# Kernel tuning notes

Measured on AMD Instinct MI355X. Metric: run time of the kernel, lower is better.

The kernel has to match this reference:

```python
import jax, jax.numpy as jnp
import numpy as np

GAMMA = 20.0
NUM_VIEWS = 64

def setup_inputs() -> dict:
    key = jax.random.key(0)
    k1, k2, k3 = jax.random.split(key, 3)
    B, L, D = 16, 4096, 1024
    v_pad = jax.random.normal(k1, (B, L, D), dtype=jnp.float32)
    v_len = jax.random.randint(k2, (B,), 1, L + 1, dtype=jnp.int32)
    # (T, H, W) per sample; only W/H ratio matters -> square 64x64 grid
    grid_thws = jnp.tile(jnp.array([[1, 64, 64]], dtype=jnp.int32), (B, 1))
    centers = jax.random.uniform(k3, (B, NUM_VIEWS, 2), dtype=jnp.float32)
    return {"v_pad": v_pad, "v_len": v_len, "grid_thws": grid_thws, "centers": centers}

def reference(v_pad, v_len, grid_thws, centers):
    B, L, D = v_pad.shape
    Lv = v_len.astype(jnp.float32)                      # [B]
    H = grid_thws[:, 1].astype(jnp.float32)
    W = grid_thws[:, 2].astype(jnp.float32)
    # adaptive 2D mapping of the 1D token sequence
    W_eff = jnp.maximum(1, jnp.round(jnp.sqrt(Lv * (W / H))).astype(jnp.int32))  # [B]
    H_eff = jnp.maximum(1, jnp.ceil(Lv / W_eff.astype(jnp.float32)).astype(jnp.int32))
    idx = jnp.arange(L, dtype=jnp.int32)                # [L]
    We = W_eff[:, None]
    He = H_eff[:, None]
    x = (idx[None, :] % We).astype(jnp.float32) / We.astype(jnp.float32)   # [B, L]
    y = (idx[None, :] // We).astype(jnp.float32) / He.astype(jnp.float32)  # [B, L]
    coords = jnp.stack([x, y], axis=-1)                 # [B, L, 2]
    # squared distance from each view center to each token coord
    diff = centers[:, :, None, :] - coords[:, None, :, :]   # [B, V, L, 2]
    dist_sq = jnp.sum(diff * diff, axis=-1)                 # [B, V, L]
    valid = (idx[None, :] < v_len[:, None]).astype(v_pad.dtype)  # [B, L]
    m = jnp.exp(-GAMMA * dist_sq) * valid[:, None, :]       # [B, V, L]
    numerator = jnp.einsum('bvl,bld->bvd', m, v_pad)        # [B, V, D]
    denominator = jnp.sum(m, axis=-1, keepdims=True) + 1e-6 # [B, V, 1]
    return numerator / denominator
```

## Files before the change

### kernel.cpp

```cpp
#include <hip/hip_runtime.h>
#include <math.h>
#include <stdint.h>


constexpr int VV      = 64;
constexpr int DC      = 128;
constexpr int KS      = 64;
constexpr int NTH     = 256;
constexpr int ST      = 134;
constexpr int SXY_MAX = 512;

typedef __attribute__((ext_vector_type(8))) short short8;
typedef __attribute__((ext_vector_type(4))) float f32x4;

static __device__ __forceinline__ unsigned short f2bf(float f) {
    unsigned u = __builtin_bit_cast(unsigned, f);
    u += 0x7fffu + ((u >> 16) & 1u);
    return (unsigned short)(u >> 16);
}

__global__ __launch_bounds__(NTH)
void dvs_mfma(const float* __restrict__ v_pad, const int* __restrict__ v_len,
              const int* __restrict__ grid_thws, const float* __restrict__ centers,
              float* __restrict__ num_part,
              float* __restrict__ den_part,
              int B, int L, int D, int K)
{
    const int kblk = blockIdx.x, dcb = blockIdx.y, b = blockIdx.z;
    const int tid  = threadIdx.x;
    const int d0   = dcb * DC;
    const int lane = tid & 63;
    const int wave = tid >> 6;

    __shared__ __align__(16) unsigned short smA[512 * 8];
    __shared__ __align__(16) unsigned short smB[KS][ST];
    __shared__ float2 sxy[SXY_MAX];
    __shared__ float  sden[4][VV];

    const int   Lv = v_len[b];
    const float Hf = (float)grid_thws[b*3 + 1];
    const float Wf = (float)grid_thws[b*3 + 2];
    const float sq = sqrtf((float)Lv * (Wf / Hf));
    int W_eff = (int)rintf(sq);                       if (W_eff < 1) W_eff = 1;
    int H_eff = (int)ceilf((float)Lv / (float)W_eff); if (H_eff < 1) H_eff = 1;
    const float invW = 1.f / (float)W_eff, invH = 1.f / (float)H_eff;

    const int chunk = (Lv + K - 1) / K;
    const int l0 = kblk * chunk;
    const int l1 = min(l0 + chunk, Lv);

    const int    av  = tid & 63;
    const int    aq  = tid >> 6;
    const float2 ctr = ((const float2*)centers)[(size_t)b * VV + av];
    const int    amf = av >> 4, ar = av & 15;
    float denacc = 0.f;

    const int sd   = tid & 31;
    const int srow = tid >> 5;

    const int fcol = lane & 15, foct = lane >> 4;

    f32x4 acc[4][2];
#pragma unroll
    for (int i = 0; i < 4; ++i) {
        acc[i][0] = f32x4{0.f, 0.f, 0.f, 0.f};
        acc[i][1] = f32x4{0.f, 0.f, 0.f, 0.f};
    }

    const float* vp_b = v_pad + (size_t)b * L * D + d0;

    for (int st = l0; st < l1; st += SXY_MAX) {
        const int st1 = min(st + SXY_MAX, l1);
        __syncthreads();

        float4 ld[8];
#pragma unroll
        for (int it = 0; it < 8; ++it) {
            const int l = st + it * 8 + srow;
            ld[it] = make_float4(0.f, 0.f, 0.f, 0.f);
            if (l < st1)
                ld[it] = *(const float4*)(vp_b + (size_t)l * D + sd * 4);
        }
        for (int i = tid; i < st1 - st; i += NTH) {
            const int l   = st + i;
            const int row = l / W_eff;
            const int col = l - row * W_eff;
            sxy[i] = make_float2((float)col * invW, (float)row * invH);
        }
        __syncthreads();

        for (int lt = st; lt < st1; lt += KS) {
#pragma unroll
            for (int it = 0; it < 8; ++it) {
                const int lrow = it * 8 + srow;
                unsigned* w = (unsigned*)&smB[lrow][sd * 4];
                w[0] = (unsigned)f2bf(ld[it].x) | ((unsigned)f2bf(ld[it].y) << 16);
                w[1] = (unsigned)f2bf(ld[it].z) | ((unsigned)f2bf(ld[it].w) << 16);
            }
#pragma unroll
            for (int ks = 0; ks < 2; ++ks) {
                union { unsigned short h[8]; short8 s; } ap;
#pragma unroll
                for (int j = 0; j < 8; ++j) {
                    const int kl = ks * 32 + aq * 8 + j;
                    const int l  = lt + kl;
                    float m = 0.f;
                    if (l < st1) {
                        const float2 xy = sxy[(lt - st) + kl];
                        const float dx = ctr.x - xy.x, dy = ctr.y - xy.y;
                        m = __expf(-20.f * (dx * dx + dy * dy));
                    }
                    denacc += m;
                    ap.h[j] = f2bf(m);
                }
                ((short8*)smA)[(ks * 4 + amf) * 64 + aq * 16 + ar] = ap.s;
            }
            __syncthreads();

            const int ltn = lt + KS;
            if (ltn < st1) {
#pragma unroll
                for (int it = 0; it < 8; ++it) {
                    const int l = ltn + it * 8 + srow;
                    ld[it] = make_float4(0.f, 0.f, 0.f, 0.f);
                    if (l < st1)
                        ld[it] = *(const float4*)(vp_b + (size_t)l * D + sd * 4);
                }
            }

#pragma unroll
            for (int ks = 0; ks < 2; ++ks) {
                short8 af[4];
#pragma unroll
                for (int mf = 0; mf < 4; ++mf)
                    af[mf] = ((const short8*)smA)[(ks * 4 + mf) * 64 + lane];

#pragma unroll
                for (int nf = 0; nf < 2; ++nf) {
                    const int colx  = wave * 32 + nf * 16 + fcol;
                    const int kbase = ks * 32 + foct * 8;
                    union { unsigned short h[8]; short8 s; } bf;
#pragma unroll
                    for (int j = 0; j < 8; ++j)
                        bf.h[j] = smB[kbase + j][colx];
#pragma unroll
                    for (int mf = 0; mf < 4; ++mf)
                        acc[mf][nf] = __builtin_amdgcn_mfma_f32_16x16x32_bf16(
                            af[mf], bf.s, acc[mf][nf], 0, 0, 0);
                }
            }
            __syncthreads();
        }
    }

    sden[aq][av] = denacc;
    __syncthreads();
    if (dcb == 0 && tid < VV) {
        den_part[((size_t)b * K + kblk) * VV + tid] =
            sden[0][tid] + sden[1][tid] + sden[2][tid] + sden[3][tid];
    }

    float* basep = num_part + ((size_t)b * K + kblk) * VV * (size_t)D + d0 + wave * 32;
#pragma unroll
    for (int mf = 0; mf < 4; ++mf) {
#pragma unroll
        for (int nf = 0; nf < 2; ++nf) {
            const int colx = nf * 16 + fcol;
            const int row0 = mf * 16 + foct * 4;
#pragma unroll
            for (int r = 0; r < 4; ++r)
                basep[(size_t)(row0 + r) * D + colx] = acc[mf][nf][r];
        }
    }
}

__global__ __launch_bounds__(256)
void dvs_reduce(const float* __restrict__ num_part,
                const float* __restrict__ den_part,
                float*       __restrict__ out,
                int B, int D, int K, int total4)
{
    const int idx = blockIdx.x * 256 + threadIdx.x;
    if (idx >= total4) return;
    const int dq4 = D / 4;
    const int d4  = idx % dq4;
    const int bv  = idx / dq4;
    const int b   = bv / VV;
    const int v   = bv - b * VV;

    float  den = 1e-6f;
    float4 num = make_float4(0.f, 0.f, 0.f, 0.f);
    for (int k = 0; k < K; ++k) {
        den += den_part[((size_t)b * K + k) * VV + v];
        const float4 p = ((const float4*)(num_part +
                          (((size_t)b * K + k) * VV + v) * (size_t)D))[d4];
        num.x += p.x; num.y += p.y; num.z += p.z; num.w += p.w;
    }
    const float inv = 1.0f / den;
    float4 o = make_float4(num.x * inv, num.y * inv, num.z * inv, num.w * inv);
    ((float4*)out)[(size_t)bv * dq4 + d4] = o;
}

extern "C" void kernel_launch(void* const* d_in, const int* in_sizes, int n_in,
                              void* d_out, int out_size, void* d_ws, size_t ws_size,
                              hipStream_t stream)
{
    const float* v_pad     = (const float*)d_in[0];
    const int*   v_len     = (const int*)d_in[1];
    const int*   grid_thws = (const int*)d_in[2];
    const float* centers   = (const float*)d_in[3];
    float*       out       = (float*)d_out;

    const int B = in_sizes[1];
    const int V = VV;
    const int D = out_size / (B * V);
    const int L = in_sizes[0] / (B * D);

    int K = 8;
    const size_t per_k = ((size_t)B * V * D + (size_t)B * V) * sizeof(float);
    while (K > 1 && (size_t)K * per_k > ws_size) K >>= 1;

    float* num_part = (float*)d_ws;
    float* den_part = num_part + (size_t)B * K * V * D;

    dim3 grid1(K, D / DC, B);
    dvs_mfma<<<grid1, NTH, 0, stream>>>(v_pad, v_len, grid_thws, centers,
                                        num_part, den_part, B, L, D, K);

    const int total4 = B * V * D / 4;
    dvs_reduce<<<(total4 + 255) / 256, 256, 0, stream>>>(num_part, den_part, out,
                                                         B, D, K, total4);
}
```

Baseline: 43.30 us.

## Split L into fixed 1024-token chunks and halve D tile per block

Replaces the per-sample even K-way split of the valid length with fixed 1024-token chunks, so blocks past v_len exit immediately and the reduce kernel sums only the chunks that exist. The D tile per block drops from 128 to 64 columns, which doubles the number of blocks along D and halves the B-tile work per wave. The aim is better load balance across samples with very different v_len and more blocks to fill the GPU. In exchange, the m-weight exp values are recomputed twice as often across D blocks, and the workspace must hold up to four partials per sample without any size check.

```diff
diff --git a/kernel.cpp b/kernel.cpp
--- a/kernel.cpp
+++ b/kernel.cpp
@@ -4,10 +4,11 @@
 
 
 constexpr int VV      = 64;
-constexpr int DC      = 128;
+constexpr int DC      = 64;
 constexpr int KS      = 64;
 constexpr int NTH     = 256;
-constexpr int ST      = 134;
+constexpr int ST2     = 66;
+constexpr int CHUNK   = 1024;
 constexpr int SXY_MAX = 512;
 
 typedef __attribute__((ext_vector_type(8))) short short8;
@@ -24,20 +25,24 @@
               const int* __restrict__ grid_thws, const float* __restrict__ centers,
               float* __restrict__ num_part,
               float* __restrict__ den_part,
-              int B, int L, int D, int K)
+              int B, int L, int D, int NKC)
 {
-    const int kblk = blockIdx.x, dcb = blockIdx.y, b = blockIdx.z;
+    const int kc = blockIdx.x, dcb = blockIdx.y, b = blockIdx.z;
+    const int Lv = v_len[b];
+    const int l0 = kc * CHUNK;
+    if (l0 >= Lv) return;
+    const int l1 = min(l0 + CHUNK, Lv);
+
     const int tid  = threadIdx.x;
     const int d0   = dcb * DC;
     const int lane = tid & 63;
     const int wave = tid >> 6;
 
-    __shared__ __align__(16) unsigned short smA[512 * 8];
-    __shared__ __align__(16) unsigned short smB[KS][ST];
+    __shared__ __align__(16) unsigned short smA[8 * 64 * 8];
+    __shared__ __align__(16) unsigned short smB[KS][ST2];
     __shared__ float2 sxy[SXY_MAX];
     __shared__ float  sden[4][VV];
 
-    const int   Lv = v_len[b];
     const float Hf = (float)grid_thws[b*3 + 1];
     const float Wf = (float)grid_thws[b*3 + 2];
     const float sq = sqrtf((float)Lv * (Wf / Hf));
@@ -45,27 +50,20 @@
     int H_eff = (int)ceilf((float)Lv / (float)W_eff); if (H_eff < 1) H_eff = 1;
     const float invW = 1.f / (float)W_eff, invH = 1.f / (float)H_eff;
 
-    const int chunk = (Lv + K - 1) / K;
-    const int l0 = kblk * chunk;
-    const int l1 = min(l0 + chunk, Lv);
-
     const int    av  = tid & 63;
     const int    aq  = tid >> 6;
     const float2 ctr = ((const float2*)centers)[(size_t)b * VV + av];
     const int    amf = av >> 4, ar = av & 15;
     float denacc = 0.f;
 
-    const int sd   = tid & 31;
-    const int srow = tid >> 5;
+    const int sd   = tid & 15;
+    const int srow = tid >> 4;
 
     const int fcol = lane & 15, foct = lane >> 4;
 
-    f32x4 acc[4][2];
-#pragma unroll
-    for (int i = 0; i < 4; ++i) {
-        acc[i][0] = f32x4{0.f, 0.f, 0.f, 0.f};
-        acc[i][1] = f32x4{0.f, 0.f, 0.f, 0.f};
-    }
+    f32x4 acc[4];
+#pragma unroll
+    for (int i = 0; i < 4; ++i) acc[i] = f32x4{0.f, 0.f, 0.f, 0.f};
 
     const float* vp_b = v_pad + (size_t)b * L * D + d0;
 
@@ -73,10 +71,10 @@
         const int st1 = min(st + SXY_MAX, l1);
         __syncthreads();
 
-        float4 ld[8];
-#pragma unroll
-        for (int it = 0; it < 8; ++it) {
-            const int l = st + it * 8 + srow;
+        float4 ld[4];
+#pragma unroll
+        for (int it = 0; it < 4; ++it) {
+            const int l = st + it * 16 + srow;
             ld[it] = make_float4(0.f, 0.f, 0.f, 0.f);
             if (l < st1)
                 ld[it] = *(const float4*)(vp_b + (size_t)l * D + sd * 4);
@@ -91,8 +89,8 @@
 
         for (int lt = st; lt < st1; lt += KS) {
 #pragma unroll
-            for (int it = 0; it < 8; ++it) {
-                const int lrow = it * 8 + srow;
+            for (int it = 0; it < 4; ++it) {
+                const int lrow = it * 16 + srow;
                 unsigned* w = (unsigned*)&smB[lrow][sd * 4];
                 w[0] = (unsigned)f2bf(ld[it].x) | ((unsigned)f2bf(ld[it].y) << 16);
                 w[1] = (unsigned)f2bf(ld[it].z) | ((unsigned)f2bf(ld[it].w) << 16);
@@ -120,8 +118,8 @@
             const int ltn = lt + KS;
             if (ltn < st1) {
 #pragma unroll
-                for (int it = 0; it < 8; ++it) {
-                    const int l = ltn + it * 8 + srow;
+                for (int it = 0; it < 4; ++it) {
+                    const int l = ltn + it * 16 + srow;
                     ld[it] = make_float4(0.f, 0.f, 0.f, 0.f);
                     if (l < st1)
                         ld[it] = *(const float4*)(vp_b + (size_t)l * D + sd * 4);
@@ -135,19 +133,15 @@
                 for (int mf = 0; mf < 4; ++mf)
                     af[mf] = ((const short8*)smA)[(ks * 4 + mf) * 64 + lane];
 
-#pragma unroll
-                for (int nf = 0; nf < 2; ++nf) {
-                    const int colx  = wave * 32 + nf * 16 + fcol;
-                    const int kbase = ks * 32 + foct * 8;
-                    union { unsigned short h[8]; short8 s; } bf;
-#pragma unroll
-                    for (int j = 0; j < 8; ++j)
-                        bf.h[j] = smB[kbase + j][colx];
-#pragma unroll
-                    for (int mf = 0; mf < 4; ++mf)
-                        acc[mf][nf] = __builtin_amdgcn_mfma_f32_16x16x32_bf16(
-                            af[mf], bf.s, acc[mf][nf], 0, 0, 0);
-                }
+                const int kbase = ks * 32 + foct * 8;
+                union { unsigned short h[8]; short8 s; } bf;
+#pragma unroll
+                for (int j = 0; j < 8; ++j)
+                    bf.h[j] = smB[kbase + j][wave * 16 + fcol];
+#pragma unroll
+                for (int mf = 0; mf < 4; ++mf)
+                    acc[mf] = __builtin_amdgcn_mfma_f32_16x16x32_bf16(
+                        af[mf], bf.s, acc[mf], 0, 0, 0);
             }
             __syncthreads();
         }
@@ -156,29 +150,26 @@
     sden[aq][av] = denacc;
     __syncthreads();
     if (dcb == 0 && tid < VV) {
-        den_part[((size_t)b * K + kblk) * VV + tid] =
+        den_part[((size_t)b * NKC + kc) * VV + tid] =
             sden[0][tid] + sden[1][tid] + sden[2][tid] + sden[3][tid];
     }
 
-    float* basep = num_part + ((size_t)b * K + kblk) * VV * (size_t)D + d0 + wave * 32;
+    float* basep = num_part + ((size_t)b * NKC + kc) * VV * (size_t)D + d0 + wave * 16;
 #pragma unroll
     for (int mf = 0; mf < 4; ++mf) {
-#pragma unroll
-        for (int nf = 0; nf < 2; ++nf) {
-            const int colx = nf * 16 + fcol;
-            const int row0 = mf * 16 + foct * 4;
-#pragma unroll
-            for (int r = 0; r < 4; ++r)
-                basep[(size_t)(row0 + r) * D + colx] = acc[mf][nf][r];
-        }
+        const int row0 = mf * 16 + foct * 4;
+#pragma unroll
+        for (int r = 0; r < 4; ++r)
+            basep[(size_t)(row0 + r) * D + fcol] = acc[mf][r];
     }
 }
 
 __global__ __launch_bounds__(256)
 void dvs_reduce(const float* __restrict__ num_part,
                 const float* __restrict__ den_part,
+                const int*   __restrict__ v_len,
                 float*       __restrict__ out,
-                int B, int D, int K, int total4)
+                int B, int D, int NKC, int total4)
 {
     const int idx = blockIdx.x * 256 + threadIdx.x;
     if (idx >= total4) return;
@@ -188,17 +179,19 @@
     const int b   = bv / VV;
     const int v   = bv - b * VV;
 
+    const int nk = (v_len[b] + CHUNK - 1) / CHUNK;
+
     float  den = 1e-6f;
     float4 num = make_float4(0.f, 0.f, 0.f, 0.f);
-    for (int k = 0; k < K; ++k) {
-        den += den_part[((size_t)b * K + k) * VV + v];
+    for (int k = 0; k < nk; ++k) {
+        den += den_part[((size_t)b * NKC + k) * VV + v];
         const float4 p = ((const float4*)(num_part +
-                          (((size_t)b * K + k) * VV + v) * (size_t)D))[d4];
+                          (((size_t)b * NKC + k) * VV + v) * (size_t)D))[d4];
         num.x += p.x; num.y += p.y; num.z += p.z; num.w += p.w;
     }
     const float inv = 1.0f / den;
-    float4 o = make_float4(num.x * inv, num.y * inv, num.z * inv, num.w * inv);
-    ((float4*)out)[(size_t)bv * dq4 + d4] = o;
+    ((float4*)out)[(size_t)bv * dq4 + d4] =
+        make_float4(num.x * inv, num.y * inv, num.z * inv, num.w * inv);
 }
 
 extern "C" void kernel_launch(void* const* d_in, const int* in_sizes, int n_in,
@@ -212,22 +205,19 @@
     float*       out       = (float*)d_out;
 
     const int B = in_sizes[1];
-    const int V = VV;
-    const int D = out_size / (B * V);
+    const int D = out_size / (B * VV);
     const int L = in_sizes[0] / (B * D);
-
-    int K = 8;
-    const size_t per_k = ((size_t)B * V * D + (size_t)B * V) * sizeof(float);
-    while (K > 1 && (size_t)K * per_k > ws_size) K >>= 1;
+    const int NKC = (L + CHUNK - 1) / CHUNK;
 
     float* num_part = (float*)d_ws;
-    float* den_part = num_part + (size_t)B * K * V * D;
-
-    dim3 grid1(K, D / DC, B);
+    float* den_part = num_part + (size_t)B * NKC * VV * D;
+
+    dim3 grid1(NKC, D / DC, B);
     dvs_mfma<<<grid1, NTH, 0, stream>>>(v_pad, v_len, grid_thws, centers,
-                                        num_part, den_part, B, L, D, K);
-
-    const int total4 = B * V * D / 4;
-    dvs_reduce<<<(total4 + 255) / 256, 256, 0, stream>>>(num_part, den_part, out,
-                                                         B, D, K, total4);
-}
+                                        num_part, den_part, B, L, D, NKC);
+
+    const int total4 = B * VV * D / 4;
+    dvs_reduce<<<(total4 + 255) / 256, 256, 0, stream>>>(num_part, den_part,
+                                                         v_len, out, B, D, NKC,
+                                                         total4);
+}
```

Result: slower. 55.80 us (+28.9%).
